# Performance work log

Measured on AMD Instinct MI355X. Metric: run time of the kernel, lower is better.

Reference implementation:

```python
import jax, jax.numpy as jnp
import numpy as np

NT, NC, D = 20000, 80000, 256
SLOPE = 0.01  # torch F.leaky_relu default negative_slope


def _lrelu(x):
    return jnp.where(x >= 0, x, SLOPE * x)


def setup_inputs() -> dict:
    key = jax.random.key(0)
    ks = jax.random.split(key, 20)
    sc = 1.0 / np.sqrt(D)

    def W(k):
        return jax.random.normal(k, (D, D), jnp.float32) * sc

    return {
        "feat_table": jax.random.normal(ks[0], (NT, D), jnp.float32),
        "feat_column": jax.random.normal(ks[1], (NC, D), jnp.float32),
        "W_t2c": W(ks[2]), "b_t2c": jnp.zeros((D,), jnp.float32),
        "W_c2t": W(ks[3]), "b_c2t": jnp.zeros((D,), jnp.float32),
        "W_c2c": W(ks[4]), "b_c2c": jnp.zeros((D,), jnp.float32),
        "W_t2t": W(ks[5]), "b_t2t": jnp.zeros((D,), jnp.float32),
        "W_h": W(ks[6]), "b_h": jnp.zeros((D,), jnp.float32),
        "src_t2c": jax.random.randint(ks[7], (320000,), 0, NT, jnp.int32),
        "dst_t2c": jax.random.randint(ks[8], (320000,), 0, NC, jnp.int32),
        "src_c2t": jax.random.randint(ks[9], (320000,), 0, NC, jnp.int32),
        "dst_c2t": jax.random.randint(ks[10], (320000,), 0, NT, jnp.int32),
        "src_c2c": jax.random.randint(ks[11], (640000,), 0, NC, jnp.int32),
        "dst_c2c": jax.random.randint(ks[12], (640000,), 0, NC, jnp.int32),
        "src_t2t": jax.random.randint(ks[13], (160000,), 0, NT, jnp.int32),
        "dst_t2t": jax.random.randint(ks[14], (160000,), 0, NT, jnp.int32),
    }


def _mean_agg(Wh, src, dst, n_dst):
    # copy_u + mean: gather src messages, segment-mean into dst nodes
    s = jax.ops.segment_sum(Wh[src], dst, num_segments=n_dst)  # [n_dst, D]
    c = jax.ops.segment_sum(jnp.ones(src.shape, Wh.dtype), dst, num_segments=n_dst)
    return s / jnp.maximum(c, 1.0)[:, None]


def reference(feat_table, feat_column,
              W_t2c, b_t2c, W_c2t, b_c2t, W_c2c, b_c2c, W_t2t, b_t2t,
              W_h, b_h,
              src_t2c, dst_t2c, src_c2t, dst_c2t,
              src_c2c, dst_c2c, src_t2t, dst_t2t):
    # per-etype Linear + leaky_relu on source-node features
    Wh_t2c = _lrelu(feat_table @ W_t2c.T + b_t2c)
    Wh_c2t = _lrelu(feat_column @ W_c2t.T + b_c2t)
    Wh_c2c = _lrelu(feat_column @ W_c2c.T + b_c2c)
    Wh_t2t = _lrelu(feat_table @ W_t2t.T + b_t2t)

    # per-etype mean aggregation, then cross-etype 'mean' (2 etypes per ntype)
    h_table = 0.5 * (_mean_agg(Wh_c2t, src_c2t, dst_c2t, NT)
                     + _mean_agg(Wh_t2t, src_t2t, dst_t2t, NT))
    h_column = 0.5 * (_mean_agg(Wh_t2c, src_t2c, dst_t2c, NC)
                      + _mean_agg(Wh_c2c, src_c2c, dst_c2c, NC))

    out_table = _lrelu(h_table @ W_h.T + b_h) + feat_table
    out_column = _lrelu(h_column @ W_h.T + b_h) + feat_column
    return out_table, out_column
```

## Files before the change

kernel.cpp:

```cpp
#include <hip/hip_runtime.h>

#define D 256
#define SLOPE 0.01f

#define BSH 9
#define BSZ 512
#define NBMAX 160
#define EPB 8192

typedef __attribute__((ext_vector_type(8))) short bf16x8;
typedef __attribute__((ext_vector_type(4))) float f32x4;

__device__ __forceinline__ float bfbits2f(unsigned int hi) {
  return __builtin_bit_cast(float, hi);
}
__device__ __forceinline__ unsigned short f2bf(float f) {
  unsigned u = __builtin_bit_cast(unsigned, f);
  u += 0x7fffu + ((u >> 16) & 1u);
  return (unsigned short)(u >> 16);
}
__device__ __forceinline__ float lrelu(float x) {
  return (x >= 0.f) ? x : SLOPE * x;
}

__device__ __forceinline__ void gld_lds16(const void* g, void* l) {
  __builtin_amdgcn_global_load_lds(
      (const __attribute__((address_space(1))) unsigned int*)g,
      (__attribute__((address_space(3))) unsigned int*)l, 16, 0, 0);
}

__global__ void cast_kernel(const float* __restrict__ in,
                            unsigned short* __restrict__ out, int n4) {
  int i = blockIdx.x * blockDim.x + threadIdx.x;
  if (i >= n4) return;
  float4 v = ((const float4*)in)[i];
  ushort4 o;
  o.x = f2bf(v.x); o.y = f2bf(v.y); o.z = f2bf(v.z); o.w = f2bf(v.w);
  ((ushort4*)out)[i] = o;
}

__global__ void cast5_kernel(const float* w0, const float* w1, const float* w2,
                             const float* w3, const float* w4,
                             unsigned short* o0, unsigned short* o1,
                             unsigned short* o2, unsigned short* o3,
                             unsigned short* o4) {
  int a = blockIdx.y;
  const float* in = a == 0 ? w0 : a == 1 ? w1 : a == 2 ? w2 : a == 3 ? w3 : w4;
  unsigned short* out = a == 0 ? o0 : a == 1 ? o1 : a == 2 ? o2 : a == 3 ? o3 : o4;
  int i = blockIdx.x * blockDim.x + threadIdx.x;
  float4 v = ((const float4*)in)[i];
  ushort4 o;
  o.x = f2bf(v.x); o.y = f2bf(v.y); o.z = f2bf(v.z); o.w = f2bf(v.w);
  ((ushort4*)out)[i] = o;
}

template <int MODE>
__device__ __forceinline__ void gemm_core(
    unsigned short* Xs, const unsigned short* __restrict__ A,
    const unsigned short* __restrict__ B, const float* __restrict__ bias,
    const float* __restrict__ residual, unsigned short* __restrict__ outb,
    float* __restrict__ outf, int M, int mblk) {
  const int t = threadIdx.x;
  const int w = t >> 6, lane = t & 63;
  const int fr = lane & 15;
  const int jb = lane >> 4;

  bf16x8 wf[4][8];
  {
    const unsigned short* wp = B + (size_t)(w * 64 + fr) * D + jb * 8;
#pragma unroll
    for (int nt = 0; nt < 4; nt++)
#pragma unroll
      for (int k0 = 0; k0 < 8; k0++)
        wf[nt][k0] = *(const bf16x8*)(wp + nt * 16 * D + k0 * 32);
  }

#pragma unroll
  for (int i = 0; i < 8; i++) {
    const int m = (i * 4 + w) * 2 + (lane >> 5);
    int row = mblk + m;
    if (row > M - 1) row = M - 1;
    const int jsrc = (lane & 31) ^ (m & 7);
    gld_lds16(A + (size_t)row * D + jsrc * 8, &Xs[(i * 4 + w) * 512]);
  }
  asm volatile("s_waitcnt vmcnt(0)" ::: "memory");
  __syncthreads();

  f32x4 acc[4][4];
#pragma unroll
  for (int i = 0; i < 4; i++)
#pragma unroll
    for (int j = 0; j < 4; j++) acc[i][j] = (f32x4){0.f, 0.f, 0.f, 0.f};

  const int r = fr & 7;
#pragma unroll
  for (int k0 = 0; k0 < 8; k0++) {
    bf16x8 xf[4];
#pragma unroll
    for (int mt = 0; mt < 4; mt++) {
      const int ml = mt * 16 + fr;
      xf[mt] = *(const bf16x8*)&Xs[ml * 256 + (((k0 * 4 + jb) ^ r) * 8)];
    }
#pragma unroll
    for (int mt = 0; mt < 4; mt++)
#pragma unroll
      for (int nt = 0; nt < 4; nt++)
        acc[mt][nt] = __builtin_amdgcn_mfma_f32_16x16x32_bf16(
            wf[nt][k0], xf[mt], acc[mt][nt], 0, 0, 0);
  }

  const int n0 = w * 64 + jb * 4;
  float4 bv[4];
#pragma unroll
  for (int nt = 0; nt < 4; nt++) bv[nt] = *(const float4*)&bias[n0 + nt * 16];

#pragma unroll
  for (int mt = 0; mt < 4; mt++) {
    const int m = mblk + mt * 16 + fr;
    if (m < M) {
      if (MODE == 1) {
        float4 rv[4];
#pragma unroll
        for (int nt = 0; nt < 4; nt++)
          rv[nt] = *(const float4*)&residual[(size_t)m * D + n0 + nt * 16];
#pragma unroll
        for (int nt = 0; nt < 4; nt++) {
          float4 o;
          o.x = lrelu(acc[mt][nt][0] + bv[nt].x) + rv[nt].x;
          o.y = lrelu(acc[mt][nt][1] + bv[nt].y) + rv[nt].y;
          o.z = lrelu(acc[mt][nt][2] + bv[nt].z) + rv[nt].z;
          o.w = lrelu(acc[mt][nt][3] + bv[nt].w) + rv[nt].w;
          *(float4*)&outf[(size_t)m * D + n0 + nt * 16] = o;
        }
      } else {
#pragma unroll
        for (int nt = 0; nt < 4; nt++) {
          ushort4 o;
          o.x = f2bf(lrelu(acc[mt][nt][0] + bv[nt].x));
          o.y = f2bf(lrelu(acc[mt][nt][1] + bv[nt].y));
          o.z = f2bf(lrelu(acc[mt][nt][2] + bv[nt].z));
          o.w = f2bf(lrelu(acc[mt][nt][3] + bv[nt].w));
          *(ushort4*)&outb[(size_t)m * D + n0 + nt * 16] = o;
        }
      }
    }
  }
}

__global__ __launch_bounds__(256, 2) void gemm0_quad(
    const unsigned short* __restrict__ A0, const unsigned short* __restrict__ A1,
    const unsigned short* __restrict__ B0, const unsigned short* __restrict__ B1,
    const unsigned short* __restrict__ B2, const unsigned short* __restrict__ B3,
    const float* b0, const float* b1, const float* b2, const float* b3,
    unsigned short* o0, unsigned short* o1, unsigned short* o2,
    unsigned short* o3, int M0, int M1) {
  __shared__ __attribute__((aligned(16))) unsigned short Xs[64 * 256];
  int a = blockIdx.y;
  const unsigned short* A = (a < 2) ? A0 : A1;
  int M = (a < 2) ? M0 : M1;
  int mblk = blockIdx.x * 64;
  if (mblk >= M) return;
  const unsigned short* B = a == 0 ? B0 : a == 1 ? B1 : a == 2 ? B2 : B3;
  const float* bias = a == 0 ? b0 : a == 1 ? b1 : a == 2 ? b2 : b3;
  unsigned short* outb = a == 0 ? o0 : a == 1 ? o1 : a == 2 ? o2 : o3;
  gemm_core<0>(Xs, A, B, bias, nullptr, outb, nullptr, M, mblk);
}

__global__ __launch_bounds__(256, 2) void gemm1_dual(
    const unsigned short* __restrict__ A0, const unsigned short* __restrict__ A1,
    const unsigned short* __restrict__ Bw, const float* bh,
    const float* __restrict__ r0, const float* __restrict__ r1,
    float* __restrict__ o0, float* __restrict__ o1, int M0, int M1) {
  __shared__ __attribute__((aligned(16))) unsigned short Xs[64 * 256];
  int a = blockIdx.y;
  const unsigned short* A = a ? A1 : A0;
  int M = a ? M1 : M0;
  int mblk = blockIdx.x * 64;
  if (mblk >= M) return;
  gemm_core<1>(Xs, A, Bw, bh, a ? r1 : r0, nullptr, a ? o1 : o0, M, mblk);
}

__global__ void hist4_kernel(const int* d0, int n0, int* c0, const int* d1,
                             int n1, int* c1, const int* d2, int n2, int* c2,
                             const int* d3, int n3, int* c3) {
  int a = blockIdx.y;
  const int* dst = a == 0 ? d0 : a == 1 ? d1 : a == 2 ? d2 : d3;
  int n = a == 0 ? n0 : a == 1 ? n1 : a == 2 ? n2 : n3;
  int* cnt = a == 0 ? c0 : a == 1 ? c1 : a == 2 ? c2 : c3;
  int i = blockIdx.x * blockDim.x + threadIdx.x;
  if (i < n) atomicAdd(&cnt[dst[i]], 1);
}

__global__ __launch_bounds__(256) void scan_p1(
    const int* c0, int n0, const int* c1, int n1, const int* c2, int n2,
    const int* c3, int n3, int* __restrict__ bsum) {
  int a = blockIdx.y;
  const int* cnt = a == 0 ? c0 : a == 1 ? c1 : a == 2 ? c2 : c3;
  int n = a == 0 ? n0 : a == 1 ? n1 : a == 2 ? n2 : n3;
  int nblk = (n + 1023) >> 10;
  int blk = blockIdx.x;
  if (blk >= nblk) return;
  int t = threadIdx.x;
  int i = (blk << 10) + t * 4;
  int s = 0;
  if (i + 3 < n) {
    int4 v = *(const int4*)(cnt + i);
    s = v.x + v.y + v.z + v.w;
  } else {
#pragma unroll
    for (int j = 0; j < 4; j++)
      if (i + j < n) s += cnt[i + j];
  }
  __shared__ int red[256];
  red[t] = s;
  __syncthreads();
  for (int off = 128; off > 0; off >>= 1) {
    if (t < off) red[t] += red[t + off];
    __syncthreads();
  }
  if (t == 0) bsum[a * 128 + blk] = red[0];
}

__global__ __launch_bounds__(128) void scan_p2(int* __restrict__ bsum, int* o0,
                                               int n0, int* o1, int n1, int* o2,
                                               int n2, int* o3, int n3) {
  int a = blockIdx.x;
  int* offs = a == 0 ? o0 : a == 1 ? o1 : a == 2 ? o2 : o3;
  int n = a == 0 ? n0 : a == 1 ? n1 : a == 2 ? n2 : n3;
  int nblk = (n + 1023) >> 10;
  int t = threadIdx.x;
  int v = (t < nblk) ? bsum[a * 128 + t] : 0;
  __shared__ int s[128];
  s[t] = v;
  __syncthreads();
  for (int off = 1; off < 128; off <<= 1) {
    int u = (t >= off) ? s[t - off] : 0;
    __syncthreads();
    s[t] += u;
    __syncthreads();
  }
  if (t < nblk) bsum[a * 128 + t] = s[t] - v;
  if (t == 127) offs[n] = s[127];
}

__global__ __launch_bounds__(256) void scan_p3(
    const int* c0, int* o0, int n0, const int* c1, int* o1, int n1,
    const int* c2, int* o2, int n2, const int* c3, int* o3, int n3,
    const int* __restrict__ bsum) {
  int a = blockIdx.y;
  const int* cnt = a == 0 ? c0 : a == 1 ? c1 : a == 2 ? c2 : c3;
  int* offs = a == 0 ? o0 : a == 1 ? o1 : a == 2 ? o2 : o3;
  int n = a == 0 ? n0 : a == 1 ? n1 : a == 2 ? n2 : n3;
  int nblk = (n + 1023) >> 10;
  int blk = blockIdx.x;
  if (blk >= nblk) return;
  int t = threadIdx.x;
  int i = (blk << 10) + t * 4;
  int4 v = {0, 0, 0, 0};
  if (i + 3 < n) {
    v = *(const int4*)(cnt + i);
  } else {
    if (i < n) v.x = cnt[i];
    if (i + 1 < n) v.y = cnt[i + 1];
    if (i + 2 < n) v.z = cnt[i + 2];
    if (i + 3 < n) v.w = cnt[i + 3];
  }
  int s = v.x + v.y + v.z + v.w;
  __shared__ int sm[256];
  sm[t] = s;
  __syncthreads();
  for (int off = 1; off < 256; off <<= 1) {
    int u = (t >= off) ? sm[t - off] : 0;
    __syncthreads();
    sm[t] += u;
    __syncthreads();
  }
  int ex = sm[t] - s + bsum[a * 128 + blk];
  int4 o;
  o.x = ex;
  o.y = ex + v.x;
  o.z = ex + v.x + v.y;
  o.w = ex + v.x + v.y + v.z;
  if (i + 3 < n) {
    *(int4*)(offs + i) = o;
  } else {
    if (i < n) offs[i] = o.x;
    if (i + 1 < n) offs[i + 1] = o.y;
    if (i + 2 < n) offs[i + 2] = o.z;
    if (i + 3 < n) offs[i + 3] = o.w;
  }
}

__global__ __launch_bounds__(256) void bucketA_kernel(
    const int* s0, const int* d0, int n0, const int* f0, int* g0, unsigned* t0, int m0,
    const int* s1, const int* d1, int n1, const int* f1, int* g1, unsigned* t1, int m1,
    const int* s2, const int* d2, int n2, const int* f2, int* g2, unsigned* t2, int m2,
    const int* s3, const int* d3, int n3, const int* f3, int* g3, unsigned* t3, int m3) {
  int a = blockIdx.y;
  const int* src = a == 0 ? s0 : a == 1 ? s1 : a == 2 ? s2 : s3;
  const int* dst = a == 0 ? d0 : a == 1 ? d1 : a == 2 ? d2 : d3;
  int n = a == 0 ? n0 : a == 1 ? n1 : a == 2 ? n2 : n3;
  const int* off = a == 0 ? f0 : a == 1 ? f1 : a == 2 ? f2 : f3;
  int* bcur = a == 0 ? g0 : a == 1 ? g1 : a == 2 ? g2 : g3;
  unsigned* temp = a == 0 ? t0 : a == 1 ? t1 : a == 2 ? t2 : t3;
  int nn = a == 0 ? m0 : a == 1 ? m1 : a == 2 ? m2 : m3;

  int blk = blockIdx.x;
  if (blk * EPB >= n) return;
  int nb = (nn + BSZ - 1) >> BSH;
  int t = threadIdx.x;
  __shared__ int cnt[NBMAX];
  __shared__ int lbase[NBMAX];
  if (t < NBMAX) cnt[t] = 0;
  __syncthreads();

  int i0 = blk * EPB + t;
#pragma unroll 4
  for (int it = 0; it < EPB / 256; it++) {
    int i = i0 + it * 256;
    if (i < n) atomicAdd(&cnt[dst[i] >> BSH], 1);
  }
  __syncthreads();
  if (t < nb) {
    int c = cnt[t];
    int g = c ? atomicAdd(&bcur[t], c) : 0;
    lbase[t] = g + off[t << BSH];
    cnt[t] = 0;
  }
  __syncthreads();
#pragma unroll 4
  for (int it = 0; it < EPB / 256; it++) {
    int i = i0 + it * 256;
    if (i < n) {
      int d = dst[i];
      int b = d >> BSH;
      int rk = atomicAdd(&cnt[b], 1);
      temp[lbase[b] + rk] = ((unsigned)src[i] << BSH) | (unsigned)(d & (BSZ - 1));
    }
  }
}

__global__ __launch_bounds__(256) void bucketB_kernel(
    const unsigned* t0, const int* f0, int* u0, int* e0, int m0,
    const unsigned* t1, const int* f1, int* u1, int* e1, int m1,
    const unsigned* t2, const int* f2, int* u2, int* e2, int m2,
    const unsigned* t3, const int* f3, int* u3, int* e3, int m3) {
  int a = blockIdx.y;
  const unsigned* temp = a == 0 ? t0 : a == 1 ? t1 : a == 2 ? t2 : t3;
  const int* off = a == 0 ? f0 : a == 1 ? f1 : a == 2 ? f2 : f3;
  int* cur = a == 0 ? u0 : a == 1 ? u1 : a == 2 ? u2 : u3;
  int* elist = a == 0 ? e0 : a == 1 ? e1 : a == 2 ? e2 : e3;
  int nn = a == 0 ? m0 : a == 1 ? m1 : a == 2 ? m2 : m3;

  int nb = (nn + BSZ - 1) >> BSH;
  int b = blockIdx.x >> 2, q = blockIdx.x & 3;
  if (b >= nb) return;
  int lo = off[b << BSH];
  int hiIdx = (b + 1) << BSH;
  if (hiIdx > nn) hiIdx = nn;
  int hi = off[hiIdx];
  int len = hi - lo;
  int chunk = (len + 3) >> 2;
  int st = lo + q * chunk;
  int en = st + chunk;
  if (en > hi) en = hi;
  for (int i = st + threadIdx.x; i < en; i += 256) {
    unsigned v = temp[i];
    int d = (b << BSH) | (int)(v & (BSZ - 1));
    int s = (int)(v >> BSH);
    int p = off[d] + atomicAdd(&cur[d], 1);
    elist[p] = s;
  }
}

__device__ __forceinline__ void add8(float* acc, uint4 p) {
  acc[0] += bfbits2f(p.x << 16);
  acc[1] += bfbits2f(p.x & 0xffff0000u);
  acc[2] += bfbits2f(p.y << 16);
  acc[3] += bfbits2f(p.y & 0xffff0000u);
  acc[4] += bfbits2f(p.z << 16);
  acc[5] += bfbits2f(p.z & 0xffff0000u);
  acc[6] += bfbits2f(p.w << 16);
  acc[7] += bfbits2f(p.w & 0xffff0000u);
}

__device__ __forceinline__ void agg_core(
    const unsigned short* __restrict__ WhA, const int* __restrict__ offsA,
    const int* __restrict__ elistA, const unsigned short* __restrict__ WhB,
    const int* __restrict__ offsB, const int* __restrict__ elistB,
    unsigned short* __restrict__ hout, int n, int wave, int lane) {
  int half = lane >> 5;
  int l32 = lane & 31;
  size_t coff = (size_t)l32 * 8;

  float accA[8] = {0, 0, 0, 0, 0, 0, 0, 0};
  float accB[8] = {0, 0, 0, 0, 0, 0, 0, 0};
  float scA, scB;

  {
    int e0 = offsA[wave], e1 = offsA[wave + 1];
    scA = 0.5f / fmaxf((float)(e1 - e0), 1.0f);
    int e = e0;
    for (; e + 8 <= e1; e += 8) {
      int s0 = elistA[e + half];
      int s1 = elistA[e + 2 + half];
      int s2 = elistA[e + 4 + half];
      int s3 = elistA[e + 6 + half];
      uint4 p0 = *(const uint4*)(WhA + (size_t)s0 * D + coff);
      uint4 p1 = *(const uint4*)(WhA + (size_t)s1 * D + coff);
      uint4 p2 = *(const uint4*)(WhA + (size_t)s2 * D + coff);
      uint4 p3 = *(const uint4*)(WhA + (size_t)s3 * D + coff);
      add8(accA, p0); add8(accA, p1); add8(accA, p2); add8(accA, p3);
    }
    for (; e + 2 <= e1; e += 2) {
      int s0 = elistA[e + half];
      uint4 p0 = *(const uint4*)(WhA + (size_t)s0 * D + coff);
      add8(accA, p0);
    }
    if (e < e1 && half == 0) {
      int s0 = elistA[e];
      uint4 p0 = *(const uint4*)(WhA + (size_t)s0 * D + coff);
      add8(accA, p0);
    }
  }
  {
    int e0 = offsB[wave], e1 = offsB[wave + 1];
    scB = 0.5f / fmaxf((float)(e1 - e0), 1.0f);
    int e = e0;
    for (; e + 8 <= e1; e += 8) {
      int s0 = elistB[e + half];
      int s1 = elistB[e + 2 + half];
      int s2 = elistB[e + 4 + half];
      int s3 = elistB[e + 6 + half];
      uint4 p0 = *(const uint4*)(WhB + (size_t)s0 * D + coff);
      uint4 p1 = *(const uint4*)(WhB + (size_t)s1 * D + coff);
      uint4 p2 = *(const uint4*)(WhB + (size_t)s2 * D + coff);
      uint4 p3 = *(const uint4*)(WhB + (size_t)s3 * D + coff);
      add8(accB, p0); add8(accB, p1); add8(accB, p2); add8(accB, p3);
    }
    for (; e + 2 <= e1; e += 2) {
      int s0 = elistB[e + half];
      uint4 p0 = *(const uint4*)(WhB + (size_t)s0 * D + coff);
      add8(accB, p0);
    }
    if (e < e1 && half == 0) {
      int s0 = elistB[e];
      uint4 p0 = *(const uint4*)(WhB + (size_t)s0 * D + coff);
      add8(accB, p0);
    }
  }

  float h[8];
#pragma unroll
  for (int j = 0; j < 8; j++) {
    h[j] = accA[j] * scA + accB[j] * scB;
    h[j] += __shfl_down(h[j], 32);
  }
  if (half == 0) {
    uint4 o;
    o.x = (unsigned)f2bf(h[0]) | ((unsigned)f2bf(h[1]) << 16);
    o.y = (unsigned)f2bf(h[2]) | ((unsigned)f2bf(h[3]) << 16);
    o.z = (unsigned)f2bf(h[4]) | ((unsigned)f2bf(h[5]) << 16);
    o.w = (unsigned)f2bf(h[6]) | ((unsigned)f2bf(h[7]) << 16);
    *(uint4*)(hout + (size_t)wave * D + coff) = o;
  }
}

__global__ __launch_bounds__(256) void aggregate2_kernel(
    const unsigned short* WhA0, const int* offsA0, const int* elA0,
    const unsigned short* WhB0, const int* offsB0, const int* elB0,
    unsigned short* h0, int n0,
    const unsigned short* WhA1, const int* offsA1, const int* elA1,
    const unsigned short* WhB1, const int* offsB1, const int* elB1,
    unsigned short* h1, int n1) {
  int a = blockIdx.y;
  int n = a ? n1 : n0;
  int wave = (blockIdx.x * 256 + threadIdx.x) >> 6;
  int lane = threadIdx.x & 63;
  if (wave >= n) return;
  if (a == 0)
    agg_core(WhA0, offsA0, elA0, WhB0, offsB0, elB0, h0, n0, wave, lane);
  else
    agg_core(WhA1, offsA1, elA1, WhB1, offsB1, elB1, h1, n1, wave, lane);
}

extern "C" void kernel_launch(void* const* d_in, const int* in_sizes, int n_in,
                              void* d_out, int out_size, void* d_ws,
                              size_t ws_size, hipStream_t stream) {
  const float* feat_table = (const float*)d_in[0];
  const float* feat_column = (const float*)d_in[1];
  const float* Wsrc[5] = {(const float*)d_in[2], (const float*)d_in[4],
                          (const float*)d_in[6], (const float*)d_in[8],
                          (const float*)d_in[10]};
  const float* b_t2c = (const float*)d_in[3];
  const float* b_c2t = (const float*)d_in[5];
  const float* b_c2c = (const float*)d_in[7];
  const float* b_t2t = (const float*)d_in[9];
  const float* b_h = (const float*)d_in[11];
  const int* src_t2c = (const int*)d_in[12];
  const int* dst_t2c = (const int*)d_in[13];
  const int* src_c2t = (const int*)d_in[14];
  const int* dst_c2t = (const int*)d_in[15];
  const int* src_c2c = (const int*)d_in[16];
  const int* dst_c2c = (const int*)d_in[17];
  const int* src_t2t = (const int*)d_in[18];
  const int* dst_t2t = (const int*)d_in[19];

  const int NT = in_sizes[0] / D;
  const int NC = in_sizes[1] / D;
  const int E_t2c = in_sizes[12], E_c2t = in_sizes[14];
  const int E_c2c = in_sizes[16], E_t2t = in_sizes[18];

  char* ws = (char*)d_ws;
  size_t cur = 0;
  auto alloc = [&](size_t bytes) -> void* {
    void* p = ws + cur;
    cur += (bytes + 255) & ~(size_t)255;
    return p;
  };
  unsigned short* Wb[5];
  for (int i = 0; i < 5; i++) Wb[i] = (unsigned short*)alloc((size_t)D * D * 2);
  unsigned short* ftb = (unsigned short*)alloc((size_t)NT * D * 2);
  unsigned short* fcb = (unsigned short*)alloc((size_t)NC * D * 2);
  unsigned short* Wh_t2c = (unsigned short*)alloc((size_t)NT * D * 2);
  unsigned short* Wh_c2t = (unsigned short*)alloc((size_t)NC * D * 2);
  unsigned short* Wh_c2c = (unsigned short*)alloc((size_t)NC * D * 2);
  unsigned short* Wh_t2t = (unsigned short*)alloc((size_t)NT * D * 2);
  size_t nints = 2 * (2 * (size_t)NT + 2 * (size_t)NC) + 4 * NBMAX;
  int* ints = (int*)alloc(sizeof(int) * nints);
  int* cnt_c2t = ints;
  int* cnt_t2t = cnt_c2t + NT;
  int* cnt_t2c = cnt_t2t + NT;
  int* cnt_c2c = cnt_t2c + NC;
  int* cur_c2t = cnt_c2c + NC;
  int* cur_t2t = cur_c2t + NT;
  int* cur_t2c = cur_t2t + NT;
  int* cur_c2c = cur_t2c + NC;
  int* bc_c2t = cur_c2c + NC;
  int* bc_t2t = bc_c2t + NBMAX;
  int* bc_t2c = bc_t2t + NBMAX;
  int* bc_c2c = bc_t2c + NBMAX;
  int* off_c2t = (int*)alloc(sizeof(int) * (NT + 1));
  int* off_t2t = (int*)alloc(sizeof(int) * (NT + 1));
  int* off_t2c = (int*)alloc(sizeof(int) * (NC + 1));
  int* off_c2c = (int*)alloc(sizeof(int) * (NC + 1));
  int* el_c2t = (int*)alloc(sizeof(int) * E_c2t);
  int* el_t2t = (int*)alloc(sizeof(int) * E_t2t);
  int* el_t2c = (int*)alloc(sizeof(int) * E_t2c);
  int* el_c2c = (int*)alloc(sizeof(int) * E_c2c);
  int* bsum = (int*)alloc(sizeof(int) * 4 * 128);

  unsigned* tp_c2t = (unsigned*)ftb;
  unsigned* tp_t2t = tp_c2t + E_c2t;
  unsigned* tp_t2c = tp_t2t + E_t2t;
  unsigned* tp_c2c = tp_t2c + E_t2c;
  unsigned short* h_tab = ftb;
  unsigned short* h_col = fcb;

  hipMemsetAsync(ints, 0, sizeof(int) * nints, stream);

  {
    dim3 g((D * D / 4 + 255) / 256, 5);
    cast5_kernel<<<g, 256, 0, stream>>>(Wsrc[0], Wsrc[1], Wsrc[2], Wsrc[3],
                                        Wsrc[4], Wb[0], Wb[1], Wb[2], Wb[3],
                                        Wb[4]);
  }
  cast_kernel<<<((NT * D / 4) + 255) / 256, 256, 0, stream>>>(feat_table, ftb,
                                                              NT * D / 4);
  cast_kernel<<<((NC * D / 4) + 255) / 256, 256, 0, stream>>>(feat_column, fcb,
                                                              NC * D / 4);

  {
    dim3 g((max(NT, NC) + 63) / 64, 4);
    gemm0_quad<<<g, 256, 0, stream>>>(ftb, fcb, Wb[0], Wb[3], Wb[1], Wb[2],
                                      b_t2c, b_t2t, b_c2t, b_c2c, Wh_t2c,
                                      Wh_t2t, Wh_c2t, Wh_c2c, NT, NC);
  }

  int Emax = max(max(E_c2t, E_t2t), max(E_t2c, E_c2c));
  {
    dim3 g((Emax + 255) / 256, 4);
    hist4_kernel<<<g, 256, 0, stream>>>(dst_c2t, E_c2t, cnt_c2t, dst_t2t,
                                        E_t2t, cnt_t2t, dst_t2c, E_t2c,
                                        cnt_t2c, dst_c2c, E_c2c, cnt_c2c);
  }
  int nmax = max(NT, NC);
  {
    dim3 g((nmax + 1023) / 1024, 4);
    scan_p1<<<g, 256, 0, stream>>>(cnt_c2t, NT, cnt_t2t, NT, cnt_t2c, NC,
                                   cnt_c2c, NC, bsum);
    scan_p2<<<4, 128, 0, stream>>>(bsum, off_c2t, NT, off_t2t, NT, off_t2c, NC,
                                   off_c2c, NC);
    scan_p3<<<g, 256, 0, stream>>>(cnt_c2t, off_c2t, NT, cnt_t2t, off_t2t, NT,
                                   cnt_t2c, off_t2c, NC, cnt_c2c, off_c2c, NC,
                                   bsum);
  }
  {
    dim3 g((Emax + EPB - 1) / EPB, 4);
    bucketA_kernel<<<g, 256, 0, stream>>>(
        src_c2t, dst_c2t, E_c2t, off_c2t, bc_c2t, tp_c2t, NT,
        src_t2t, dst_t2t, E_t2t, off_t2t, bc_t2t, tp_t2t, NT,
        src_t2c, dst_t2c, E_t2c, off_t2c, bc_t2c, tp_t2c, NC,
        src_c2c, dst_c2c, E_c2c, off_c2c, bc_c2c, tp_c2c, NC);
  }
  {
    int nbmax = (max(NT, NC) + BSZ - 1) >> BSH;
    dim3 g(nbmax * 4, 4);
    bucketB_kernel<<<g, 256, 0, stream>>>(
        tp_c2t, off_c2t, cur_c2t, el_c2t, NT,
        tp_t2t, off_t2t, cur_t2t, el_t2t, NT,
        tp_t2c, off_t2c, cur_t2c, el_t2c, NC,
        tp_c2c, off_c2c, cur_c2c, el_c2c, NC);
  }

  {
    dim3 g((max(NT, NC) + 3) / 4, 2);
    aggregate2_kernel<<<g, 256, 0, stream>>>(
        Wh_c2t, off_c2t, el_c2t, Wh_t2t, off_t2t, el_t2t, h_tab, NT,
        Wh_t2c, off_t2c, el_t2c, Wh_c2c, off_c2c, el_c2c, h_col, NC);
  }

  float* out_tab = (float*)d_out;
  float* out_col = out_tab + (size_t)NT * D;
  {
    dim3 g((max(NT, NC) + 63) / 64, 2);
    gemm1_dual<<<g, 256, 0, stream>>>(h_tab, h_col, Wb[4], b_h, feat_table,
                                      feat_column, out_tab, out_col, NT, NC);
  }
}
```

Baseline: 611.5 us.

## Build CSR via bucket-level counting and per-bucket local sort, dropping global histogram

Replaces the per-node global histogram plus three-pass scan with a bucket-level count, a single-block bucket scan, and a final per-bucket kernel that computes node offsets and scatters edges using shared-memory counters. This removes global atomics on per-node counters and the large memset of count/cursor arrays. The aggregation is also split from one two-ntype launch into two separate launches, one per node type. The risk is lower parallelism in the final kernel, which now uses one block per bucket instead of four, and serialized launches for aggregation.

```diff
diff --git a/kernel.cpp b/kernel.cpp
--- a/kernel.cpp
+++ b/kernel.cpp
@@ -180,140 +180,18 @@
   gemm_core<1>(Xs, A, Bw, bh, a ? r1 : r0, nullptr, a ? o1 : o0, M, mblk);
 }
 
-__global__ void hist4_kernel(const int* d0, int n0, int* c0, const int* d1,
-                             int n1, int* c1, const int* d2, int n2, int* c2,
-                             const int* d3, int n3, int* c3) {
+__global__ __launch_bounds__(256) void bucketCount_kernel(
+    const int* d0, int n0, const int* d1, int n1, const int* d2, int n2,
+    const int* d3, int n3, int* __restrict__ bcnt) {
   int a = blockIdx.y;
   const int* dst = a == 0 ? d0 : a == 1 ? d1 : a == 2 ? d2 : d3;
   int n = a == 0 ? n0 : a == 1 ? n1 : a == 2 ? n2 : n3;
-  int* cnt = a == 0 ? c0 : a == 1 ? c1 : a == 2 ? c2 : c3;
-  int i = blockIdx.x * blockDim.x + threadIdx.x;
-  if (i < n) atomicAdd(&cnt[dst[i]], 1);
-}
-
-__global__ __launch_bounds__(256) void scan_p1(
-    const int* c0, int n0, const int* c1, int n1, const int* c2, int n2,
-    const int* c3, int n3, int* __restrict__ bsum) {
-  int a = blockIdx.y;
-  const int* cnt = a == 0 ? c0 : a == 1 ? c1 : a == 2 ? c2 : c3;
-  int n = a == 0 ? n0 : a == 1 ? n1 : a == 2 ? n2 : n3;
-  int nblk = (n + 1023) >> 10;
-  int blk = blockIdx.x;
-  if (blk >= nblk) return;
-  int t = threadIdx.x;
-  int i = (blk << 10) + t * 4;
-  int s = 0;
-  if (i + 3 < n) {
-    int4 v = *(const int4*)(cnt + i);
-    s = v.x + v.y + v.z + v.w;
-  } else {
-#pragma unroll
-    for (int j = 0; j < 4; j++)
-      if (i + j < n) s += cnt[i + j];
-  }
-  __shared__ int red[256];
-  red[t] = s;
-  __syncthreads();
-  for (int off = 128; off > 0; off >>= 1) {
-    if (t < off) red[t] += red[t + off];
-    __syncthreads();
-  }
-  if (t == 0) bsum[a * 128 + blk] = red[0];
-}
-
-__global__ __launch_bounds__(128) void scan_p2(int* __restrict__ bsum, int* o0,
-                                               int n0, int* o1, int n1, int* o2,
-                                               int n2, int* o3, int n3) {
-  int a = blockIdx.x;
-  int* offs = a == 0 ? o0 : a == 1 ? o1 : a == 2 ? o2 : o3;
-  int n = a == 0 ? n0 : a == 1 ? n1 : a == 2 ? n2 : n3;
-  int nblk = (n + 1023) >> 10;
-  int t = threadIdx.x;
-  int v = (t < nblk) ? bsum[a * 128 + t] : 0;
-  __shared__ int s[128];
-  s[t] = v;
-  __syncthreads();
-  for (int off = 1; off < 128; off <<= 1) {
-    int u = (t >= off) ? s[t - off] : 0;
-    __syncthreads();
-    s[t] += u;
-    __syncthreads();
-  }
-  if (t < nblk) bsum[a * 128 + t] = s[t] - v;
-  if (t == 127) offs[n] = s[127];
-}
-
-__global__ __launch_bounds__(256) void scan_p3(
-    const int* c0, int* o0, int n0, const int* c1, int* o1, int n1,
-    const int* c2, int* o2, int n2, const int* c3, int* o3, int n3,
-    const int* __restrict__ bsum) {
-  int a = blockIdx.y;
-  const int* cnt = a == 0 ? c0 : a == 1 ? c1 : a == 2 ? c2 : c3;
-  int* offs = a == 0 ? o0 : a == 1 ? o1 : a == 2 ? o2 : o3;
-  int n = a == 0 ? n0 : a == 1 ? n1 : a == 2 ? n2 : n3;
-  int nblk = (n + 1023) >> 10;
-  int blk = blockIdx.x;
-  if (blk >= nblk) return;
-  int t = threadIdx.x;
-  int i = (blk << 10) + t * 4;
-  int4 v = {0, 0, 0, 0};
-  if (i + 3 < n) {
-    v = *(const int4*)(cnt + i);
-  } else {
-    if (i < n) v.x = cnt[i];
-    if (i + 1 < n) v.y = cnt[i + 1];
-    if (i + 2 < n) v.z = cnt[i + 2];
-    if (i + 3 < n) v.w = cnt[i + 3];
-  }
-  int s = v.x + v.y + v.z + v.w;
-  __shared__ int sm[256];
-  sm[t] = s;
-  __syncthreads();
-  for (int off = 1; off < 256; off <<= 1) {
-    int u = (t >= off) ? sm[t - off] : 0;
-    __syncthreads();
-    sm[t] += u;
-    __syncthreads();
-  }
-  int ex = sm[t] - s + bsum[a * 128 + blk];
-  int4 o;
-  o.x = ex;
-  o.y = ex + v.x;
-  o.z = ex + v.x + v.y;
-  o.w = ex + v.x + v.y + v.z;
-  if (i + 3 < n) {
-    *(int4*)(offs + i) = o;
-  } else {
-    if (i < n) offs[i] = o.x;
-    if (i + 1 < n) offs[i + 1] = o.y;
-    if (i + 2 < n) offs[i + 2] = o.z;
-    if (i + 3 < n) offs[i + 3] = o.w;
-  }
-}
-
-__global__ __launch_bounds__(256) void bucketA_kernel(
-    const int* s0, const int* d0, int n0, const int* f0, int* g0, unsigned* t0, int m0,
-    const int* s1, const int* d1, int n1, const int* f1, int* g1, unsigned* t1, int m1,
-    const int* s2, const int* d2, int n2, const int* f2, int* g2, unsigned* t2, int m2,
-    const int* s3, const int* d3, int n3, const int* f3, int* g3, unsigned* t3, int m3) {
-  int a = blockIdx.y;
-  const int* src = a == 0 ? s0 : a == 1 ? s1 : a == 2 ? s2 : s3;
-  const int* dst = a == 0 ? d0 : a == 1 ? d1 : a == 2 ? d2 : d3;
-  int n = a == 0 ? n0 : a == 1 ? n1 : a == 2 ? n2 : n3;
-  const int* off = a == 0 ? f0 : a == 1 ? f1 : a == 2 ? f2 : f3;
-  int* bcur = a == 0 ? g0 : a == 1 ? g1 : a == 2 ? g2 : g3;
-  unsigned* temp = a == 0 ? t0 : a == 1 ? t1 : a == 2 ? t2 : t3;
-  int nn = a == 0 ? m0 : a == 1 ? m1 : a == 2 ? m2 : m3;
-
   int blk = blockIdx.x;
   if (blk * EPB >= n) return;
-  int nb = (nn + BSZ - 1) >> BSH;
   int t = threadIdx.x;
   __shared__ int cnt[NBMAX];
-  __shared__ int lbase[NBMAX];
   if (t < NBMAX) cnt[t] = 0;
   __syncthreads();
-
   int i0 = blk * EPB + t;
 #pragma unroll 4
   for (int it = 0; it < EPB / 256; it++) {
@@ -321,10 +199,70 @@
     if (i < n) atomicAdd(&cnt[dst[i] >> BSH], 1);
   }
   __syncthreads();
-  if (t < nb) {
+  if (t < NBMAX && cnt[t]) atomicAdd(&bcnt[a * NBMAX + t], cnt[t]);
+}
+
+__global__ __launch_bounds__(256) void bucketScan_kernel(
+    const int* __restrict__ bcnt, int* __restrict__ bbase,
+    int* o0, int n0, int e0, int* o1, int n1, int e1,
+    int* o2, int n2, int e2, int* o3, int n3, int e3) {
+  __shared__ int s[256];
+  int t = threadIdx.x;
+  for (int a = 0; a < 4; a++) {
+    int v = (t < NBMAX) ? bcnt[a * NBMAX + t] : 0;
+    s[t] = v;
+    __syncthreads();
+    for (int off = 1; off < 256; off <<= 1) {
+      int u = (t >= off) ? s[t - off] : 0;
+      __syncthreads();
+      s[t] += u;
+      __syncthreads();
+    }
+    if (t <= NBMAX) {
+      int ex = (t < NBMAX) ? (s[t] - ((t < NBMAX) ? bcnt[a * NBMAX + t] : 0))
+                           : s[NBMAX - 1];
+      if (t < NBMAX)
+        bbase[a * (NBMAX + 1) + t] = s[t] - v;
+      else
+        bbase[a * (NBMAX + 1) + NBMAX] = s[NBMAX - 1];
+      (void)ex;
+    }
+    __syncthreads();
+  }
+  if (t == 0) { o0[n0] = e0; o1[n1] = e1; o2[n2] = e2; o3[n3] = e3; }
+}
+
+__global__ __launch_bounds__(256) void bucketA_kernel(
+    const int* s0, const int* d0, int n0, unsigned* t0,
+    const int* s1, const int* d1, int n1, unsigned* t1,
+    const int* s2, const int* d2, int n2, unsigned* t2,
+    const int* s3, const int* d3, int n3, unsigned* t3,
+    const int* __restrict__ bbase, int* __restrict__ bcur) {
+  int a = blockIdx.y;
+  const int* src = a == 0 ? s0 : a == 1 ? s1 : a == 2 ? s2 : s3;
+  const int* dst = a == 0 ? d0 : a == 1 ? d1 : a == 2 ? d2 : d3;
+  int n = a == 0 ? n0 : a == 1 ? n1 : a == 2 ? n2 : n3;
+  unsigned* temp = a == 0 ? t0 : a == 1 ? t1 : a == 2 ? t2 : t3;
+
+  int blk = blockIdx.x;
+  if (blk * EPB >= n) return;
+  int t = threadIdx.x;
+  __shared__ int cnt[NBMAX];
+  __shared__ int lbase[NBMAX];
+  if (t < NBMAX) cnt[t] = 0;
+  __syncthreads();
+
+  int i0 = blk * EPB + t;
+#pragma unroll 4
+  for (int it = 0; it < EPB / 256; it++) {
+    int i = i0 + it * 256;
+    if (i < n) atomicAdd(&cnt[dst[i] >> BSH], 1);
+  }
+  __syncthreads();
+  if (t < NBMAX) {
     int c = cnt[t];
-    int g = c ? atomicAdd(&bcur[t], c) : 0;
-    lbase[t] = g + off[t << BSH];
+    int g = c ? atomicAdd(&bcur[a * NBMAX + t], c) : 0;
+    lbase[t] = g + bbase[a * (NBMAX + 1) + t];
     cnt[t] = 0;
   }
   __syncthreads();
@@ -340,36 +278,58 @@
   }
 }
 
-__global__ __launch_bounds__(256) void bucketB_kernel(
-    const unsigned* t0, const int* f0, int* u0, int* e0, int m0,
-    const unsigned* t1, const int* f1, int* u1, int* e1, int m1,
-    const unsigned* t2, const int* f2, int* u2, int* e2, int m2,
-    const unsigned* t3, const int* f3, int* u3, int* e3, int m3) {
+__global__ __launch_bounds__(256) void bucketFinal_kernel(
+    const unsigned* t0, int* o0, int* e0, int m0,
+    const unsigned* t1, int* o1, int* e1, int m1,
+    const unsigned* t2, int* o2, int* e2, int m2,
+    const unsigned* t3, int* o3, int* e3, int m3,
+    const int* __restrict__ bbase) {
   int a = blockIdx.y;
   const unsigned* temp = a == 0 ? t0 : a == 1 ? t1 : a == 2 ? t2 : t3;
-  const int* off = a == 0 ? f0 : a == 1 ? f1 : a == 2 ? f2 : f3;
-  int* cur = a == 0 ? u0 : a == 1 ? u1 : a == 2 ? u2 : u3;
+  int* offs = a == 0 ? o0 : a == 1 ? o1 : a == 2 ? o2 : o3;
   int* elist = a == 0 ? e0 : a == 1 ? e1 : a == 2 ? e2 : e3;
   int nn = a == 0 ? m0 : a == 1 ? m1 : a == 2 ? m2 : m3;
 
   int nb = (nn + BSZ - 1) >> BSH;
-  int b = blockIdx.x >> 2, q = blockIdx.x & 3;
+  int b = blockIdx.x;
   if (b >= nb) return;
-  int lo = off[b << BSH];
-  int hiIdx = (b + 1) << BSH;
-  if (hiIdx > nn) hiIdx = nn;
-  int hi = off[hiIdx];
-  int len = hi - lo;
-  int chunk = (len + 3) >> 2;
-  int st = lo + q * chunk;
-  int en = st + chunk;
-  if (en > hi) en = hi;
-  for (int i = st + threadIdx.x; i < en; i += 256) {
+  int lo = bbase[a * (NBMAX + 1) + b];
+  int hi = bbase[a * (NBMAX + 1) + b + 1];
+  int t = threadIdx.x;
+
+  __shared__ int cnt[BSZ];
+  __shared__ int psum[BSZ];
+  __shared__ int sm[256];
+  cnt[t] = 0; cnt[t + 256] = 0;
+  __syncthreads();
+  for (int i = lo + t; i < hi; i += 256)
+    atomicAdd(&cnt[temp[i] & (BSZ - 1)], 1);
+  __syncthreads();
+  int c0 = cnt[2 * t], c1 = cnt[2 * t + 1];
+  int s = c0 + c1;
+  sm[t] = s;
+  __syncthreads();
+  for (int off = 1; off < 256; off <<= 1) {
+    int u = (t >= off) ? sm[t - off] : 0;
+    __syncthreads();
+    sm[t] += u;
+    __syncthreads();
+  }
+  int ex = sm[t] - s;
+  psum[2 * t] = ex;
+  psum[2 * t + 1] = ex + c0;
+  cnt[2 * t] = 0; cnt[2 * t + 1] = 0;
+  __syncthreads();
+
+  int node0 = b << BSH;
+  if (node0 + 2 * t < nn) offs[node0 + 2 * t] = lo + psum[2 * t];
+  if (node0 + 2 * t + 1 < nn) offs[node0 + 2 * t + 1] = lo + psum[2 * t + 1];
+
+  for (int i = lo + t; i < hi; i += 256) {
     unsigned v = temp[i];
-    int d = (b << BSH) | (int)(v & (BSZ - 1));
-    int s = (int)(v >> BSH);
-    int p = off[d] + atomicAdd(&cur[d], 1);
-    elist[p] = s;
+    int d = v & (BSZ - 1);
+    int rk = atomicAdd(&cnt[d], 1);
+    elist[lo + psum[d] + rk] = (int)(v >> BSH);
   }
 }
 
@@ -384,11 +344,14 @@
   acc[7] += bfbits2f(p.w & 0xffff0000u);
 }
 
-__device__ __forceinline__ void agg_core(
+__global__ __launch_bounds__(256) void aggregate_kernel(
     const unsigned short* __restrict__ WhA, const int* __restrict__ offsA,
     const int* __restrict__ elistA, const unsigned short* __restrict__ WhB,
     const int* __restrict__ offsB, const int* __restrict__ elistB,
-    unsigned short* __restrict__ hout, int n, int wave, int lane) {
+    unsigned short* __restrict__ hout, int n) {
+  int wave = (blockIdx.x * 256 + threadIdx.x) >> 6;
+  int lane = threadIdx.x & 63;
+  if (wave >= n) return;
   int half = lane >> 5;
   int l32 = lane & 31;
   size_t coff = (size_t)l32 * 8;
@@ -464,24 +427,6 @@
     o.w = (unsigned)f2bf(h[6]) | ((unsigned)f2bf(h[7]) << 16);
     *(uint4*)(hout + (size_t)wave * D + coff) = o;
   }
-}
-
-__global__ __launch_bounds__(256) void aggregate2_kernel(
-    const unsigned short* WhA0, const int* offsA0, const int* elA0,
-    const unsigned short* WhB0, const int* offsB0, const int* elB0,
-    unsigned short* h0, int n0,
-    const unsigned short* WhA1, const int* offsA1, const int* elA1,
-    const unsigned short* WhB1, const int* offsB1, const int* elB1,
-    unsigned short* h1, int n1) {
-  int a = blockIdx.y;
-  int n = a ? n1 : n0;
-  int wave = (blockIdx.x * 256 + threadIdx.x) >> 6;
-  int lane = threadIdx.x & 63;
-  if (wave >= n) return;
-  if (a == 0)
-    agg_core(WhA0, offsA0, elA0, WhB0, offsB0, elB0, h0, n0, wave, lane);
-  else
-    agg_core(WhA1, offsA1, elA1, WhB1, offsB1, elB1, h1, n1, wave, lane);
 }
 
 extern "C" void kernel_launch(void* const* d_in, const int* in_sizes, int n_in,
@@ -526,20 +471,9 @@
   unsigned short* Wh_c2t = (unsigned short*)alloc((size_t)NC * D * 2);
   unsigned short* Wh_c2c = (unsigned short*)alloc((size_t)NC * D * 2);
   unsigned short* Wh_t2t = (unsigned short*)alloc((size_t)NT * D * 2);
-  size_t nints = 2 * (2 * (size_t)NT + 2 * (size_t)NC) + 4 * NBMAX;
-  int* ints = (int*)alloc(sizeof(int) * nints);
-  int* cnt_c2t = ints;
-  int* cnt_t2t = cnt_c2t + NT;
-  int* cnt_t2c = cnt_t2t + NT;
-  int* cnt_c2c = cnt_t2c + NC;
-  int* cur_c2t = cnt_c2c + NC;
-  int* cur_t2t = cur_c2t + NT;
-  int* cur_t2c = cur_t2t + NT;
-  int* cur_c2c = cur_t2c + NC;
-  int* bc_c2t = cur_c2c + NC;
-  int* bc_t2t = bc_c2t + NBMAX;
-  int* bc_t2c = bc_t2t + NBMAX;
-  int* bc_c2c = bc_t2c + NBMAX;
+  int* bcnt = (int*)alloc(sizeof(int) * 2 * 4 * NBMAX);
+  int* bcur = bcnt + 4 * NBMAX;
+  int* bbase = (int*)alloc(sizeof(int) * 4 * (NBMAX + 1));
   int* off_c2t = (int*)alloc(sizeof(int) * (NT + 1));
   int* off_t2t = (int*)alloc(sizeof(int) * (NT + 1));
   int* off_t2c = (int*)alloc(sizeof(int) * (NC + 1));
@@ -548,7 +482,6 @@
   int* el_t2t = (int*)alloc(sizeof(int) * E_t2t);
   int* el_t2c = (int*)alloc(sizeof(int) * E_t2c);
   int* el_c2c = (int*)alloc(sizeof(int) * E_c2c);
-  int* bsum = (int*)alloc(sizeof(int) * 4 * 128);
 
   unsigned* tp_c2t = (unsigned*)ftb;
   unsigned* tp_t2t = tp_c2t + E_c2t;
@@ -557,7 +490,7 @@
   unsigned short* h_tab = ftb;
   unsigned short* h_col = fcb;
 
-  hipMemsetAsync(ints, 0, sizeof(int) * nints, stream);
+  hipMemsetAsync(bcnt, 0, sizeof(int) * 2 * 4 * NBMAX, stream);
 
   {
     dim3 g((D * D / 4 + 255) / 256, 5);
@@ -579,46 +512,33 @@
 
   int Emax = max(max(E_c2t, E_t2t), max(E_t2c, E_c2c));
   {
-    dim3 g((Emax + 255) / 256, 4);
-    hist4_kernel<<<g, 256, 0, stream>>>(dst_c2t, E_c2t, cnt_c2t, dst_t2t,
-                                        E_t2t, cnt_t2t, dst_t2c, E_t2c,
-                                        cnt_t2c, dst_c2c, E_c2c, cnt_c2c);
-  }
-  int nmax = max(NT, NC);
-  {
-    dim3 g((nmax + 1023) / 1024, 4);
-    scan_p1<<<g, 256, 0, stream>>>(cnt_c2t, NT, cnt_t2t, NT, cnt_t2c, NC,
-                                   cnt_c2c, NC, bsum);
-    scan_p2<<<4, 128, 0, stream>>>(bsum, off_c2t, NT, off_t2t, NT, off_t2c, NC,
-                                   off_c2c, NC);
-    scan_p3<<<g, 256, 0, stream>>>(cnt_c2t, off_c2t, NT, cnt_t2t, off_t2t, NT,
-                                   cnt_t2c, off_t2c, NC, cnt_c2c, off_c2c, NC,
-                                   bsum);
-  }
+    dim3 g((Emax + EPB - 1) / EPB, 4);
+    bucketCount_kernel<<<g, 256, 0, stream>>>(dst_c2t, E_c2t, dst_t2t, E_t2t,
+                                              dst_t2c, E_t2c, dst_c2c, E_c2c,
+                                              bcnt);
+  }
+  bucketScan_kernel<<<1, 256, 0, stream>>>(
+      bcnt, bbase, off_c2t, NT, E_c2t, off_t2t, NT, E_t2t, off_t2c, NC, E_t2c,
+      off_c2c, NC, E_c2c);
   {
     dim3 g((Emax + EPB - 1) / EPB, 4);
     bucketA_kernel<<<g, 256, 0, stream>>>(
-        src_c2t, dst_c2t, E_c2t, off_c2t, bc_c2t, tp_c2t, NT,
-        src_t2t, dst_t2t, E_t2t, off_t2t, bc_t2t, tp_t2t, NT,
-        src_t2c, dst_t2c, E_t2c, off_t2c, bc_t2c, tp_t2c, NC,
-        src_c2c, dst_c2c, E_c2c, off_c2c, bc_c2c, tp_c2c, NC);
+        src_c2t, dst_c2t, E_c2t, tp_c2t, src_t2t, dst_t2t, E_t2t, tp_t2t,
+        src_t2c, dst_t2c, E_t2c, tp_t2c, src_c2c, dst_c2c, E_c2c, tp_c2c,
+        bbase, bcur);
   }
   {
     int nbmax = (max(NT, NC) + BSZ - 1) >> BSH;
-    dim3 g(nbmax * 4, 4);
-    bucketB_kernel<<<g, 256, 0, stream>>>(
-        tp_c2t, off_c2t, cur_c2t, el_c2t, NT,
-        tp_t2t, off_t2t, cur_t2t, el_t2t, NT,
-        tp_t2c, off_t2c, cur_t2c, el_t2c, NC,
-        tp_c2c, off_c2c, cur_c2c, el_c2c, NC);
-  }
-
-  {
-    dim3 g((max(NT, NC) + 3) / 4, 2);
-    aggregate2_kernel<<<g, 256, 0, stream>>>(
-        Wh_c2t, off_c2t, el_c2t, Wh_t2t, off_t2t, el_t2t, h_tab, NT,
-        Wh_t2c, off_t2c, el_t2c, Wh_c2c, off_c2c, el_c2c, h_col, NC);
-  }
+    dim3 g(nbmax, 4);
+    bucketFinal_kernel<<<g, 256, 0, stream>>>(
+        tp_c2t, off_c2t, el_c2t, NT, tp_t2t, off_t2t, el_t2t, NT,
+        tp_t2c, off_t2c, el_t2c, NC, tp_c2c, off_c2c, el_c2c, NC, bbase);
+  }
+
+  aggregate_kernel<<<(NC + 3) / 4, 256, 0, stream>>>(
+      Wh_t2c, off_t2c, el_t2c, Wh_c2c, off_c2c, el_c2c, h_col, NC);
+  aggregate_kernel<<<(NT + 3) / 4, 256, 0, stream>>>(
+      Wh_c2t, off_c2t, el_c2t, Wh_t2t, off_t2t, el_t2t, h_tab, NT);
 
   float* out_tab = (float*)d_out;
   float* out_col = out_tab + (size_t)NT * D;
```

New measurement: 536.3 us. 1.14x faster.
